# Kernel optimization log

Hardware: AMD Instinct MI355X
Metric: run time of the kernel (lower is better)

The kernel has to match this reference:

```python
import jax, jax.numpy as jnp
import numpy as np

ALPHA = 0.2  # LeakyReLU negative slope
NEG_INF = -1e9


def setup_inputs() -> dict:
    key = jax.random.key(0)
    k1, k2, k3, k4 = jax.random.split(key, 4)
    B, N, F_in, F_out = 4, 4096, 128, 128
    h = jax.random.normal(k1, (B, N, F_in), dtype=jnp.float32)
    adj = jax.random.randint(k2, (B, N, N), 0, 2, dtype=jnp.int32)
    # Xavier-uniform init matching nn.Linear weights
    limW = np.sqrt(6.0 / (F_in + F_out))
    W = jax.random.uniform(k3, (F_in, F_out), jnp.float32, -limW, limW)
    lima = np.sqrt(6.0 / (2 * F_out + 1))
    a = jax.random.uniform(k4, (2 * F_out,), jnp.float32, -lima, lima)
    return {"h": h, "adj": adj, "W": W, "a": a}


def reference(h, adj, W, a):
    # h: (B, N, F_in), adj: (B, N, N) int, W: (F_in, F_out), a: (2*F_out,)
    F_out = W.shape[1]
    Wh = jnp.einsum("bnf,fo->bno", h, W)  # (B, N, F_out)
    a_i, a_j = a[:F_out], a[F_out:]
    # e_ij = leakyrelu(a . [Wh_i, Wh_j]) = leakyrelu(a_i.Wh_i + a_j.Wh_j)
    si = Wh @ a_i  # (B, N) contribution of destination node i
    sj = Wh @ a_j  # (B, N) contribution of source node j
    e = si[:, :, None] + sj[:, None, :]  # (B, N, N)
    e = jnp.where(e > 0, e, ALPHA * e)  # LeakyReLU
    e = jnp.where(adj > 0, e, NEG_INF)  # masked scores
    attention = jax.nn.softmax(e, axis=-1)  # (B, N, N)
    # dropout is identity in eval mode
    h_prime = jnp.einsum("bij,bjo->bio", attention, Wh)  # (B, N, F_out)
    return jax.nn.elu(h_prime)  # concat=True -> ELU
```

## Files before the change

### kernel.cpp

```cpp
#include <hip/hip_runtime.h>

#define GN 4096
#define GF 128
#define GB 4

typedef __attribute__((ext_vector_type(8))) short short8;
typedef __attribute__((ext_vector_type(4))) float floatx4;
typedef __attribute__((ext_vector_type(2))) int intx2;

static __device__ __forceinline__ unsigned short f2bf(float x){
  unsigned int u = __float_as_uint(x);
  u += 0x7FFFu + ((u >> 16) & 1u);
  return (unsigned short)(u >> 16);
}


__global__ __launch_bounds__(256)
void gat_prep(const float* __restrict__ h, const float* __restrict__ W,
              const float* __restrict__ a, unsigned short* __restrict__ whB,
              float* __restrict__ si_g, unsigned short* __restrict__ EFh)
{
  __shared__ float hl[16*GF];
  __shared__ float red[2][2][16];
  const int tid = threadIdx.x;
  const int b   = blockIdx.x >> 8;
  const int r0  = (blockIdx.x & 255) << 4;
  const int o = tid & 127, g = tid >> 7;

  const float4* hb4 = (const float4*)(h + ((size_t)(b*GN + r0))*GF);
  ((float4*)hl)[tid]       = hb4[tid];
  ((float4*)hl)[tid + 256] = hb4[tid + 256];
  __syncthreads();

  float acc[8];
  #pragma unroll
  for (int r=0;r<8;++r) acc[r] = 0.f;
  const float* Wp = W + o;
  for (int f4=0; f4<32; ++f4){
    const float w0 = Wp[(f4*4+0)*GF];
    const float w1 = Wp[(f4*4+1)*GF];
    const float w2 = Wp[(f4*4+2)*GF];
    const float w3 = Wp[(f4*4+3)*GF];
    #pragma unroll
    for (int r=0;r<8;++r){
      const float4 h4 = *(const float4*)&hl[((g<<3)+r)*GF + (f4<<2)];
      acc[r] = fmaf(h4.x, w0, acc[r]);
      acc[r] = fmaf(h4.y, w1, acc[r]);
      acc[r] = fmaf(h4.z, w2, acc[r]);
      acc[r] = fmaf(h4.w, w3, acc[r]);
    }
  }

  const float ai = a[o], aj = a[GF + o];
  const int lane = tid & 63, wh = (tid >> 6) & 1;
  #pragma unroll
  for (int r=0;r<8;++r){
    float vi = acc[r]*ai, vj = acc[r]*aj;
    #pragma unroll
    for (int off=32; off; off>>=1){ vi += __shfl_down(vi, off); vj += __shfl_down(vj, off); }
    if (lane == 0){ red[0][wh][(g<<3)+r] = vi; red[1][wh][(g<<3)+r] = vj; }
  }

  unsigned short us[8] __attribute__((aligned(16)));
  #pragma unroll
  for (int r=0;r<8;++r) us[r] = f2bf(acc[r]);
  {
    const int j0 = r0 + (g<<3);
    const int Je = (j0 & ~127) + ((j0 & 127) >> 1);
    unsigned short ev[4] __attribute__((aligned(8))) = {us[0],us[2],us[4],us[6]};
    unsigned short od[4] __attribute__((aligned(8))) = {us[1],us[3],us[5],us[7]};
    unsigned short* d0 = whB + (((size_t)(b*128 + (Je>>5))*128 + o)<<5) + (Je&31);
    *(uint2*)d0          = *(const uint2*)ev;
    *(uint2*)(d0 + 8192) = *(const uint2*)od;
  }

  __syncthreads();
  if (tid < 16){
    si_g[b*GN + r0 + tid] = red[0][0][tid] + red[0][1][tid];
  } else if (tid < 32){
    const int r = tid - 16;
    const int jj = r0 + r;
    const int J  = (jj & ~127) + ((jj & 1) << 6) + ((jj & 127) >> 1);
    const float vsj = red[1][0][r] + red[1][1][r];
    EFh[(size_t)b*8192 + J]        = f2bf(__expf(vsj));
    EFh[(size_t)b*8192 + 4096 + J] = f2bf(__expf(0.2f*vsj));
  }
}

__global__ __launch_bounds__(256, 2)
void gat_main(const int* __restrict__ adj, const unsigned short* __restrict__ whB,
              const float* __restrict__ si_g, const unsigned short* __restrict__ EFh,
              float* __restrict__ out)
{
  __shared__ __align__(16) char smem[34304];
  unsigned short* sEj = (unsigned short*)smem;
  unsigned long long* bits64 = (unsigned long long*)(smem + 16384);
  float* smemc = (float*)smem;

  const int tid  = threadIdx.x;
  const int wave = tid >> 6, lane = tid & 63;
  const int b  = (blockIdx.x >> 1) & 3;
  const int i0 = ((((blockIdx.x >> 3) << 1) | (blockIdx.x & 1))) << 5;
  const int m = lane & 15, quad = lane >> 4, q8 = quad << 3;
  const int jw = wave << 10, jw32 = wave << 5;
  const int rrot = wave << 3;

  const intx2* adjb2 = (const intx2*)(adj + ((size_t)(b*GN + i0))*GN + jw) + lane;

#define LOADVV(vv_, sc_) do { \
    _Pragma("unroll") \
    for (int r=0;r<32;++r){ \
      const int rr = (r + rrot) & 31; \
      vv_[r] = __builtin_nontemporal_load(adjb2 + ((sc_)<<6) + rr*(GN/2)); \
    } \
  } while(0)

  intx2 vv[32];
  LOADVV(vv, 0);

  const float si0 = si_g[(size_t)b*GN + i0 + m];
  const float si1 = si_g[(size_t)b*GN + i0 + 16 + m];
  const float Ri0 = __expf(-0.8f*si0), Ri1 = __expf(-0.8f*si1);
  const unsigned short* lanebase = whB + ((size_t)b<<19) + (m<<5) + q8;

  {
    const uint4* Eg = (const uint4*)(EFh + (size_t)b*8192);
    uint4* sE4 = (uint4*)sEj;
    #pragma unroll
    for (int k=0;k<4;++k) sE4[tid + (k<<8)] = Eg[tid + (k<<8)];
  }

  floatx4 acc0[8], acc1[8];
  #pragma unroll
  for (int c=0;c<8;++c){ acc0[c] = (floatx4){0.f,0.f,0.f,0.f}; acc1[c] = (floatx4){0.f,0.f,0.f,0.f}; }
  floatx4 lf0 = (floatx4){0.f,0.f,0.f,0.f}, lf1 = (floatx4){0.f,0.f,0.f,0.f};
  const short8 ones8 = {0x3F80,0x3F80,0x3F80,0x3F80,0x3F80,0x3F80,0x3F80,0x3F80};

#define BALLOTS(vv_, scdst_) do { \
    unsigned long long* bw = bits64 + (((wave<<1) | ((scdst_)&1)) << 6); \
    _Pragma("unroll") \
    for (int r=0;r<32;++r){ \
      const int rr = (r + rrot) & 31; \
      const unsigned long long m0 = __ballot(vv_[r].x > 0); \
      const unsigned long long m1 = __ballot(vv_[r].y > 0); \
      if (lane == 0){ bw[(rr<<1)] = m0; bw[(rr<<1)|1] = m1; } \
    } \
    asm volatile("s_waitcnt lgkmcnt(0)" ::: "memory"); \
  } while(0)

#define BCLOAD(Bc_, chunk_) do { \
    const unsigned short* wb = lanebase + ((size_t)(jw32 + ((chunk_)<<1)) << 12); \
    _Pragma("unroll") \
    for (int c=0;c<8;++c) Bc_[c]   = *(const short8*)(wb + (c<<9)); \
    _Pragma("unroll") \
    for (int c=0;c<8;++c) Bc_[8+c] = *(const short8*)(wb + 4096 + (c<<9)); \
  } while(0)

#define COMPUTE_CH(sc_, k_, Bc_) do { \
    const unsigned int* bwp = (const unsigned int*)(bits64 + (((wave<<1) | ((sc_)&1)) << 6)); \
    _Pragma("unroll") \
    for (int t=0;t<2;++t){ \
      const unsigned int sh0 = bwp[(m<<2)|((k_)<<1)|t] >> q8; \
      const unsigned int sh1 = bwp[((m+16)<<2)|((k_)<<1)|t] >> q8; \
      const int jj = jw + ((sc_)<<7) + ((k_)<<6) + (t<<5) + q8; \
      const short8 Es = *(const short8*)&sEj[jj]; \
      const short8 Fs = *(const short8*)&sEj[4096 + jj]; \
      const unsigned int* Eu = (const unsigned int*)&Es; \
      const unsigned int* Fu = (const unsigned int*)&Fs; \
      unsigned int aw0[4], aw1[4]; \
      _Pragma("unroll") \
      for (int p=0;p<4;++p){ \
        const float E0 = __uint_as_float(Eu[p] << 16); \
        const float E1 = __uint_as_float(Eu[p] & 0xFFFF0000u); \
        const float F0 = __uint_as_float(Fu[p] << 16); \
        const float F1 = __uint_as_float(Fu[p] & 0xFFFF0000u); \
        const float p00 = fmaxf(E0, Ri0*F0), p01 = fmaxf(E1, Ri0*F1); \
        const float p10 = fmaxf(E0, Ri1*F0), p11 = fmaxf(E1, Ri1*F1); \
        unsigned int w0, w1; \
        asm("v_cvt_pk_bf16_f32 %0, %1, %2" : "=v"(w0) : "v"(p00), "v"(p01)); \
        asm("v_cvt_pk_bf16_f32 %0, %1, %2" : "=v"(w1) : "v"(p10), "v"(p11)); \
        const unsigned int k00 = (unsigned int)(((int)(sh0 << (31-2*p))) >> 31); \
        const unsigned int k01 = (unsigned int)(((int)(sh0 << (30-2*p))) >> 31); \
        const unsigned int k10 = (unsigned int)(((int)(sh1 << (31-2*p))) >> 31); \
        const unsigned int k11 = (unsigned int)(((int)(sh1 << (30-2*p))) >> 31); \
        aw0[p] = w0 & ((k00 & 0xFFFFu) | (k01 << 16)); \
        aw1[p] = w1 & ((k10 & 0xFFFFu) | (k11 << 16)); \
      } \
      const short8 af0 = *(const short8*)aw0; \
      const short8 af1 = *(const short8*)aw1; \
      _Pragma("unroll") \
      for (int c=0;c<8;++c){ \
        acc0[c] = __builtin_amdgcn_mfma_f32_16x16x32_bf16(af0, Bc_[(t<<3)+c], acc0[c], 0, 0, 0); \
        acc1[c] = __builtin_amdgcn_mfma_f32_16x16x32_bf16(af1, Bc_[(t<<3)+c], acc1[c], 0, 0, 0); \
      } \
      lf0 = __builtin_amdgcn_mfma_f32_16x16x32_bf16(af0, ones8, lf0, 0, 0, 0); \
      lf1 = __builtin_amdgcn_mfma_f32_16x16x32_bf16(af1, ones8, lf1, 0, 0, 0); \
    } \
  } while(0)

  __syncthreads();

  BALLOTS(vv, 0);

  #pragma unroll 1
  for (int sc = 0; sc < 7; ++sc){
    {
      short8 Bc[16];
      BCLOAD(Bc, (sc<<1));
      LOADVV(vv, sc+1);
      COMPUTE_CH(sc, 0, Bc);
    }
    {
      short8 Bc[16];
      BCLOAD(Bc, (sc<<1)|1);
      COMPUTE_CH(sc, 1, Bc);
    }
    BALLOTS(vv, sc+1);
  }
  { short8 Bc[16]; BCLOAD(Bc, 14); COMPUTE_CH(7, 0, Bc); }
  { short8 Bc[16]; BCLOAD(Bc, 15); COMPUTE_CH(7, 1, Bc); }

#undef COMPUTE_CH
#undef BCLOAD
#undef BALLOTS
#undef LOADVV

  #pragma unroll 1
  for (int g = 0; g < 2; ++g){
    __syncthreads();
    #pragma unroll
    for (int c=0;c<8;++c){
      #pragma unroll
      for (int r=0;r<4;++r){
        const float v = g ? acc1[c][r] : acc0[c][r];
        smemc[(wave*16 + quad*4 + r)*132 + c*16 + m] = v;
      }
    }
    if (m == 0){
      #pragma unroll
      for (int r=0;r<4;++r) smemc[8448 + wave*16 + quad*4 + r] = g ? lf1[r] : lf0[r];
    }
    __syncthreads();

    const int rr = tid >> 5;
    const int c4 = (tid & 31) << 2;
    #pragma unroll
    for (int hh = 0; hh < 2; ++hh){
      const int row = rr + (hh<<3);
      const float l = smemc[8448+row] + smemc[8448+16+row]
                    + smemc[8448+32+row] + smemc[8448+48+row];
      const float rl = __builtin_amdgcn_rcpf(l);
      float4 o4;
      #pragma unroll
      for (int k=0;k<4;++k){
        const int col = c4 + k;
        const float s = smemc[row*132+col] + smemc[(16+row)*132+col]
                      + smemc[(32+row)*132+col] + smemc[(48+row)*132+col];
        float v = s * rl;
        v = v > 0.f ? v : expm1f(v);
        ((float*)&o4)[k] = v;
      }
      *(float4*)&out[((size_t)(b*GN + i0 + (g<<4) + row))*GF + c4] = o4;
    }
  }
}

extern "C" void kernel_launch(void* const* d_in, const int* in_sizes, int n_in,
                              void* d_out, int out_size, void* d_ws, size_t ws_size,
                              hipStream_t stream)
{
  (void)in_sizes; (void)n_in; (void)out_size; (void)ws_size;
  const float* h   = (const float*)d_in[0];
  const int*   adj = (const int*)d_in[1];
  const float* W   = (const float*)d_in[2];
  const float* a   = (const float*)d_in[3];
  float* out = (float*)d_out;

  char* ws = (char*)d_ws;
  unsigned short* whB   = (unsigned short*)ws;
  float*          si    = (float*)(ws + (size_t)4*1024*1024);
  unsigned short* EFh   = (unsigned short*)(ws + (size_t)4*1024*1024 + 64*1024);

  gat_prep<<<GB*GN/16, 256, 0, stream>>>(h, W, a, whB, si, EFh);
  gat_main<<<GB*GN/32, 256, 0, stream>>>(adj, whB, si, EFh, out);
}
```

Measured before the change: 397.2 us.

## Widen adjacency loads to 16-byte vectors and re-permute Wh/E layout to match

Adjacency rows are now loaded as int4 (16 bytes per lane) instead of int2, so each super-chunk covers 256 columns, with four ballots per load and a bitmask buffer twice as large. The prep kernel's interleaved layout for Wh (bf16) and the exp tables is changed from a 2-way to a 4-way column permutation so the MFMA operands line up with the new bit ordering. The main loop is restructured into 3 iterations of 4 chunks, with the adjacency loads split into two half-batches that are issued and balloted mid-iteration. The intent is fewer, wider global loads on the dominant adjacency stream. The cost is more register pressure from the two 16-entry int4 arrays and a doubled bitmask in LDS, whose layout against the fixed 34304-byte smem allocation is not verified here.

Result: slower. 411.7 us (+3.7%).

```diff
diff --git a/kernel.cpp b/kernel.cpp
--- a/kernel.cpp
+++ b/kernel.cpp
@@ -6,7 +6,7 @@
 
 typedef __attribute__((ext_vector_type(8))) short short8;
 typedef __attribute__((ext_vector_type(4))) float floatx4;
-typedef __attribute__((ext_vector_type(2))) int intx2;
+typedef __attribute__((ext_vector_type(4))) int intx4;
 
 static __device__ __forceinline__ unsigned short f2bf(float x){
   unsigned int u = __float_as_uint(x);
@@ -66,12 +66,13 @@
   for (int r=0;r<8;++r) us[r] = f2bf(acc[r]);
   {
     const int j0 = r0 + (g<<3);
-    const int Je = (j0 & ~127) + ((j0 & 127) >> 1);
-    unsigned short ev[4] __attribute__((aligned(8))) = {us[0],us[2],us[4],us[6]};
-    unsigned short od[4] __attribute__((aligned(8))) = {us[1],us[3],us[5],us[7]};
-    unsigned short* d0 = whB + (((size_t)(b*128 + (Je>>5))*128 + o)<<5) + (Je&31);
-    *(uint2*)d0          = *(const uint2*)ev;
-    *(uint2*)(d0 + 8192) = *(const uint2*)od;
+    const int Jb = (j0 & ~255) + ((j0 & 255) >> 2);
+    unsigned short* d0 = whB + (((size_t)(b*128 + (Jb>>5))*128 + o)<<5) + (Jb&31);
+    #pragma unroll
+    for (int c=0;c<4;++c){
+      const unsigned int w = (unsigned int)us[c] | ((unsigned int)us[c+4] << 16);
+      *(unsigned int*)(d0 + 8192*c) = w;
+    }
   }
 
   __syncthreads();
@@ -80,7 +81,7 @@
   } else if (tid < 32){
     const int r = tid - 16;
     const int jj = r0 + r;
-    const int J  = (jj & ~127) + ((jj & 1) << 6) + ((jj & 127) >> 1);
+    const int J  = (jj & ~255) + ((jj & 3) << 6) + ((jj & 255) >> 2);
     const float vsj = red[1][0][r] + red[1][1][r];
     EFh[(size_t)b*8192 + J]        = f2bf(__expf(vsj));
     EFh[(size_t)b*8192 + 4096 + J] = f2bf(__expf(0.2f*vsj));
@@ -105,18 +106,20 @@
   const int jw = wave << 10, jw32 = wave << 5;
   const int rrot = wave << 3;
 
-  const intx2* adjb2 = (const intx2*)(adj + ((size_t)(b*GN + i0))*GN + jw) + lane;
-
-#define LOADVV(vv_, sc_) do { \
-    _Pragma("unroll") \
-    for (int r=0;r<32;++r){ \
-      const int rr = (r + rrot) & 31; \
-      vv_[r] = __builtin_nontemporal_load(adjb2 + ((sc_)<<6) + rr*(GN/2)); \
+  const intx4* adjb4 = (const intx4*)(adj + ((size_t)(b*GN + i0))*GN + jw) + lane;
+
+#define LOADVV(vv_, sc_, h_) do { \
+    _Pragma("unroll") \
+    for (int r=0;r<16;++r){ \
+      const int rr = (r + rrot + ((h_)<<4)) & 31; \
+      vv_[r] = __builtin_nontemporal_load(adjb4 + ((sc_)<<6) + rr*(GN/4)); \
     } \
   } while(0)
 
-  intx2 vv[32];
-  LOADVV(vv, 0);
+  intx4 vv[16];
+  LOADVV(vv, 0, 0);
+  intx4 vp[16];
+  LOADVV(vp, 0, 1);
 
   const float si0 = si_g[(size_t)b*GN + i0 + m];
   const float si1 = si_g[(size_t)b*GN + i0 + 16 + m];
@@ -136,20 +139,25 @@
   floatx4 lf0 = (floatx4){0.f,0.f,0.f,0.f}, lf1 = (floatx4){0.f,0.f,0.f,0.f};
   const short8 ones8 = {0x3F80,0x3F80,0x3F80,0x3F80,0x3F80,0x3F80,0x3F80,0x3F80};
 
-#define BALLOTS(vv_, scdst_) do { \
-    unsigned long long* bw = bits64 + (((wave<<1) | ((scdst_)&1)) << 6); \
-    _Pragma("unroll") \
-    for (int r=0;r<32;++r){ \
-      const int rr = (r + rrot) & 31; \
+#define BALLOTS(vv_, scdst_, h_) do { \
+    unsigned long long* bw = bits64 + (((wave<<1) | ((scdst_)&1)) << 7); \
+    _Pragma("unroll") \
+    for (int r=0;r<16;++r){ \
+      const int rr = (r + rrot + ((h_)<<4)) & 31; \
       const unsigned long long m0 = __ballot(vv_[r].x > 0); \
       const unsigned long long m1 = __ballot(vv_[r].y > 0); \
-      if (lane == 0){ bw[(rr<<1)] = m0; bw[(rr<<1)|1] = m1; } \
+      const unsigned long long m2 = __ballot(vv_[r].z > 0); \
+      const unsigned long long m3 = __ballot(vv_[r].w > 0); \
+      if (lane == 0){ \
+        bw[(rr<<2)]   = m0; bw[(rr<<2)|1] = m1; \
+        bw[(rr<<2)|2] = m2; bw[(rr<<2)|3] = m3; \
+      } \
     } \
     asm volatile("s_waitcnt lgkmcnt(0)" ::: "memory"); \
   } while(0)
 
-#define BCLOAD(Bc_, chunk_) do { \
-    const unsigned short* wb = lanebase + ((size_t)(jw32 + ((chunk_)<<1)) << 12); \
+#define BCLOAD(Bc_, ch_) do { \
+    const unsigned short* wb = lanebase + ((size_t)(jw32 + ((ch_)<<1)) << 12); \
     _Pragma("unroll") \
     for (int c=0;c<8;++c) Bc_[c]   = *(const short8*)(wb + (c<<9)); \
     _Pragma("unroll") \
@@ -157,12 +165,12 @@
   } while(0)
 
 #define COMPUTE_CH(sc_, k_, Bc_) do { \
-    const unsigned int* bwp = (const unsigned int*)(bits64 + (((wave<<1) | ((sc_)&1)) << 6)); \
+    const unsigned int* bwp = (const unsigned int*)(bits64 + (((wave<<1) | ((sc_)&1)) << 7)); \
     _Pragma("unroll") \
     for (int t=0;t<2;++t){ \
-      const unsigned int sh0 = bwp[(m<<2)|((k_)<<1)|t] >> q8; \
-      const unsigned int sh1 = bwp[((m+16)<<2)|((k_)<<1)|t] >> q8; \
-      const int jj = jw + ((sc_)<<7) + ((k_)<<6) + (t<<5) + q8; \
+      const unsigned int sh0 = bwp[(m<<3)|((k_)<<1)|t] >> q8; \
+      const unsigned int sh1 = bwp[((m+16)<<3)|((k_)<<1)|t] >> q8; \
+      const int jj = jw + ((sc_)<<8) + ((k_)<<6) + (t<<5) + q8; \
       const short8 Es = *(const short8*)&sEj[jj]; \
       const short8 Fs = *(const short8*)&sEj[4096 + jj]; \
       const unsigned int* Eu = (const unsigned int*)&Es; \
@@ -200,25 +208,22 @@
 
   __syncthreads();
 
-  BALLOTS(vv, 0);
+  BALLOTS(vv, 0, 0);
+  BALLOTS(vp, 0, 1);
 
   #pragma unroll 1
-  for (int sc = 0; sc < 7; ++sc){
-    {
-      short8 Bc[16];
-      BCLOAD(Bc, (sc<<1));
-      LOADVV(vv, sc+1);
-      COMPUTE_CH(sc, 0, Bc);
-    }
-    {
-      short8 Bc[16];
-      BCLOAD(Bc, (sc<<1)|1);
-      COMPUTE_CH(sc, 1, Bc);
-    }
-    BALLOTS(vv, sc+1);
-  }
-  { short8 Bc[16]; BCLOAD(Bc, 14); COMPUTE_CH(7, 0, Bc); }
-  { short8 Bc[16]; BCLOAD(Bc, 15); COMPUTE_CH(7, 1, Bc); }
+  for (int sc = 0; sc < 3; ++sc){
+    { short8 Bc[16]; BCLOAD(Bc, (sc<<2)|0); LOADVV(vv, sc+1, 0); COMPUTE_CH(sc, 0, Bc); }
+    { short8 Bc[16]; BCLOAD(Bc, (sc<<2)|1); COMPUTE_CH(sc, 1, Bc); }
+    BALLOTS(vv, sc+1, 0);
+    { short8 Bc[16]; BCLOAD(Bc, (sc<<2)|2); LOADVV(vv, sc+1, 1); COMPUTE_CH(sc, 2, Bc); }
+    { short8 Bc[16]; BCLOAD(Bc, (sc<<2)|3); COMPUTE_CH(sc, 3, Bc); }
+    BALLOTS(vv, sc+1, 1);
+  }
+  { short8 Bc[16]; BCLOAD(Bc, 12); COMPUTE_CH(3, 0, Bc); }
+  { short8 Bc[16]; BCLOAD(Bc, 13); COMPUTE_CH(3, 1, Bc); }
+  { short8 Bc[16]; BCLOAD(Bc, 14); COMPUTE_CH(3, 2, Bc); }
+  { short8 Bc[16]; BCLOAD(Bc, 15); COMPUTE_CH(3, 3, Bc); }
 
 #undef COMPUTE_CH
 #undef BCLOAD
```
